# Kernel tuning notes

Hardware: AMD Instinct MI355X
Metric: run time of the kernel (lower is better)

## Reference

```python
import jax, jax.numpy as jnp
import numpy as np

N_FFT = 2048
HOP = 441
WIN_SIZE = 7
PAD = WIN_SIZE // 2
NP_WIN = WIN_SIZE * WIN_SIZE
COV_NORM = NP_WIN / (NP_WIN - 1.0)  # sample covariance, skimage default
DATA_RANGE = 2.0  # skimage float dtype_range (-1,1)
C1 = (0.01 * DATA_RANGE) ** 2
C2 = (0.03 * DATA_RANGE) ** 2
EPS = 1e-8

# periodic hann window (librosa fftbins=True)
_HANN = 0.5 - 0.5 * np.cos(2.0 * np.pi * np.arange(N_FFT) / N_FFT)


def wav_to_spectrogram(x):
    # x: [B, C, S] -> magnitude spectrogram [B, C, T, F]
    pad = N_FFT // 2
    xp = jnp.pad(x, ((0, 0), (0, 0), (pad, pad)), mode='reflect')  # torch 'reflect'
    L = xp.shape[-1]
    n_frames = (L - N_FFT) // HOP + 1
    idx = jnp.arange(n_frames)[:, None] * HOP + jnp.arange(N_FFT)[None, :]
    frames = xp[..., idx] * jnp.asarray(_HANN, xp.dtype)  # [B,C,T,N_FFT]
    spec = jnp.fft.rfft(frames, axis=-1)
    mag = jnp.sqrt(jnp.maximum(spec.real ** 2 + spec.imag ** 2, EPS))
    return mag


def _umean_last(x):
    # 1D uniform mean filter (size 7) along last axis, scipy 'reflect' boundary
    xp = jnp.pad(x, [(0, 0)] * (x.ndim - 1) + [(PAD, PAD)], mode='symmetric')
    cs = jnp.cumsum(xp, axis=-1)
    zero = jnp.zeros(cs.shape[:-1] + (1,), cs.dtype)
    cs = jnp.concatenate([zero, cs], axis=-1)
    return (cs[..., WIN_SIZE:] - cs[..., :-WIN_SIZE]) / WIN_SIZE


def umean2d(x):
    # separable 7x7 uniform filter over last two axes
    x = _umean_last(x)
    x = jnp.swapaxes(_umean_last(jnp.swapaxes(x, -1, -2)), -1, -2)
    return x


def ssim_map_mean(X, Y):
    ux, uy = umean2d(X), umean2d(Y)
    uxx, uyy, uxy = umean2d(X * X), umean2d(Y * Y), umean2d(X * Y)
    vx = COV_NORM * (uxx - ux * ux)
    vy = COV_NORM * (uyy - uy * uy)
    vxy = COV_NORM * (uxy - ux * uy)
    S = ((2 * ux * uy + C1) * (2 * vxy + C2)) / ((ux * ux + uy * uy + C1) * (vx + vy + C2))
    # crop pad on each side (skimage) then mean over the spatial map
    return jnp.mean(S[..., PAD:-PAD, PAD:-PAD], axis=(-2, -1))


def setup_inputs() -> dict:
    key = jax.random.key(0)
    k1, k2 = jax.random.split(key)
    B, C, S = 32, 2, 176400
    output = jax.random.normal(k1, (B, C, S), dtype=jnp.float32)
    target = jax.random.normal(k2, (B, C, S), dtype=jnp.float32)
    return {"output": output, "target": target}


def reference(output, target):
    so = wav_to_spectrogram(output)
    st = wav_to_spectrogram(target)
    res = ssim_map_mean(so, st)  # [B, C]
    return res[..., None, None]  # [B, C, 1, 1]
```

## Files before the change

### kernel.cpp

```cpp
#include <hip/hip_runtime.h>
#include <math.h>

#ifndef M_PI
#define M_PI 3.14159265358979323846
#endif

constexpr int S_LEN    = 176400;
constexpr int NFFT     = 2048;
constexpr int NC       = 1024;
constexpr int HOP_     = 441;
constexpr int T_FRAMES = 401;
constexpr int F_BINS   = 1025;
constexpr int F_STRIDE = 1028;
constexpr int N_CH     = 64;
constexpr float EPS_   = 1e-8f;
constexpr float C1_    = 0.0004f;
constexpr float C2_    = 0.0036f;
constexpr float COV_NORM_ = 49.0f / 48.0f;

constexpr int WIN_OFF  = 0;
constexpr int TWG_OFF  = 2048;
constexpr int UTW_OFF  = 3584;
constexpr int SPEC_OFF = 5696;
constexpr int RPB_     = 10;
constexpr int N_CHUNKS = 40;

__device__ __forceinline__ int phys(int i) { return i ^ ((i >> 2) & 15) ^ ((i >> 6) & 15); }

__device__ __forceinline__ float2 cadd(float2 a, float2 b){ return make_float2(a.x+b.x, a.y+b.y); }
__device__ __forceinline__ float2 csub(float2 a, float2 b){ return make_float2(a.x-b.x, a.y-b.y); }
__device__ __forceinline__ float2 cmul(float2 a, float2 b){ return make_float2(a.x*b.x-a.y*b.y, a.x*b.y+a.y*b.x); }

__global__ __launch_bounds__(256) void init_tables_kernel(float* __restrict__ ws, float* __restrict__ out) {
    const int idx = blockIdx.x * 256 + threadIdx.x;
    if (idx < 64) out[idx] = 0.0f;
    if (idx < NFFT) {
        ws[WIN_OFF + idx] = 0.5f - 0.5f * cosf((float)(2.0 * M_PI / NFFT) * (float)idx);
    }
    if (idx < 768) {
        float ang = -2.0f * (float)M_PI * (float)idx / (float)NC;
        float s, c; sincosf(ang, &s, &c);
        ws[TWG_OFF + 2*idx] = c; ws[TWG_OFF + 2*idx+1] = s;
    }
    if (idx < F_BINS) {
        float ang = -(float)M_PI * (float)idx / (float)NC;
        float s, c; sincosf(ang, &s, &c);
        ws[UTW_OFF + 2*idx] = c; ws[UTW_OFF + 2*idx+1] = s;
    }
}

__device__ __forceinline__ void r4_dif_inplace(
    float2* __restrict__ A, int r0, int r1, int r2, int r3,
    float2 w1, float2 w2, float2 w3, bool tw)
{
    float2 x0c = A[r0];
    float2 x1c = A[r1];
    float2 x2c = A[r2];
    float2 x3c = A[r3];

    float2 a = cadd(x0c, x2c);
    float2 b = csub(x0c, x2c);
    float2 c = cadd(x1c, x3c);
    float2 d = csub(x1c, x3c);

    float2 y0 = cadd(a, c);
    float2 y2 = csub(a, c);
    float2 y1 = make_float2(b.x + d.y, b.y - d.x);
    float2 y3 = make_float2(b.x - d.y, b.y + d.x);

    A[r0] = y0;
    A[r1] = tw ? cmul(y1, w1) : y1;
    A[r2] = tw ? cmul(y2, w2) : y2;
    A[r3] = tw ? cmul(y3, w3) : y3;
}

__global__ __launch_bounds__(256, 8) void stft_mag_kernel(
    const float* __restrict__ x0, const float* __restrict__ x1,
    float* __restrict__ ws, int ch0, int nch, int swizzle)
{
    __shared__ float2 buf[2 * NC];

    const int tid = threadIdx.x;

    int ch, t;
    if (swizzle) {
        int g = blockIdx.x;
        ch = ch0 + (g & 7) * 8 + ((g >> 3) & 7);
        t  = g >> 6;
    } else {
        t  = blockIdx.x;
        ch = ch0 + blockIdx.y;
    }

    const float* __restrict__ xin0 = x0 + (size_t)ch * S_LEN;
    const float* __restrict__ xin1 = x1 + (size_t)ch * S_LEN;
    const float*  __restrict__ win = ws + WIN_OFF;
    const float2* __restrict__ twg = (const float2*)(ws + TWG_OFF);
    const float2* __restrict__ utw = (const float2*)(ws + UTW_OFF);

    const int base = t * HOP_ - NFFT / 2;
    float* fA0 = (float*)buf;
    float* fA1 = (float*)(buf + NC);
    if (base >= 0 && base + NFFT <= S_LEN) {
        #pragma unroll
        for (int k = 0; k < NFFT / 256; ++k) {
            int n = k * 256 + tid;
            int j = base + n;
            float w = win[n];
            int p = 2 * phys(n >> 1) + (n & 1);
            fA0[p] = xin0[j] * w;
            fA1[p] = xin1[j] * w;
        }
    } else {
        #pragma unroll
        for (int k = 0; k < NFFT / 256; ++k) {
            int n = k * 256 + tid;
            int j = base + n;
            j = (j < 0) ? -j : j;
            j = (j >= S_LEN) ? (2 * S_LEN - 2 - j) : j;
            float w = win[n];
            int p = 2 * phys(n >> 1) + (n & 1);
            fA0[p] = xin0[j] * w;
            fA1[p] = xin1[j] * w;
        }
    }
    __syncthreads();

    #pragma unroll
    for (int s = 0; s < 5; ++s) {
        const int M  = 256 >> (2 * s);
        const int q  = tid & (M - 1);
        const int e  = q << (2 * s);
        const int i0 = 4 * (tid - q) + q;

        const int r0 = phys(i0);
        const int r1 = phys(i0 + M);
        const int r2 = phys(i0 + 2 * M);
        const int r3 = phys(i0 + 3 * M);

        float2 w1, w2, w3;
        if (s < 4) {
            w1 = twg[e];
            w2 = twg[2 * e];
            w3 = twg[3 * e];
        } else {
            w1 = w2 = w3 = make_float2(1.0f, 0.0f);
        }

        r4_dif_inplace(buf,      r0, r1, r2, r3, w1, w2, w3, s < 4);
        r4_dif_inplace(buf + NC, r0, r1, r2, r3, w1, w2, w3, s < 4);

        __syncthreads();
    }

    const size_t perT = (size_t)T_FRAMES * F_STRIDE;
    float* __restrict__ sout0 =
        ws + SPEC_OFF + (size_t)(ch - ch0) * perT + (size_t)t * F_STRIDE;
    float* __restrict__ sout1 = sout0 + (size_t)nch * perT;

    const int R8 = ((tid & 3) << 6) | ((tid & 12) << 2) | ((tid >> 2) & 12) | ((tid >> 6) & 3);

    #pragma unroll
    for (int k = 0; k < 5; ++k) {
        int r = k * 256 + tid;
        if (k < 4 || tid == 0) {
            const int ra = (k < 4) ? ((R8 << 2) | k) : 0;
            const int rn = (NC - r) & (NC - 1);
            const int rb = ((rn & 3) << 8) | ((rn & 12) << 4) | (rn & 48)
                         | ((rn >> 4) & 12) | ((rn >> 8) & 3);
            const int ia = phys(ra);
            const int ib = phys(rb);
            float2 wu = utw[r];

            {
                float2 Zr = buf[ia];
                float2 Zn = buf[ib];
                float Ex = 0.5f * (Zr.x + Zn.x);
                float Ey = 0.5f * (Zr.y - Zn.y);
                float Ox = 0.5f * (Zr.y + Zn.y);
                float Oy = 0.5f * (Zn.x - Zr.x);
                float Xx = Ex + wu.x * Ox - wu.y * Oy;
                float Xy = Ey + wu.x * Oy + wu.y * Ox;
                sout0[r] = sqrtf(fmaxf(Xx * Xx + Xy * Xy, EPS_));
            }
            {
                float2 Zr = buf[NC + ia];
                float2 Zn = buf[NC + ib];
                float Ex = 0.5f * (Zr.x + Zn.x);
                float Ey = 0.5f * (Zr.y - Zn.y);
                float Ox = 0.5f * (Zr.y + Zn.y);
                float Oy = 0.5f * (Zn.x - Zr.x);
                float Xx = Ex + wu.x * Ox - wu.y * Oy;
                float Xy = Ey + wu.x * Oy + wu.y * Ox;
                sout1[r] = sqrtf(fmaxf(Xx * Xx + Xy * Xy, EPS_));
            }
        }
    }
}

__global__ __launch_bounds__(256) void ssim_kernel(
    const float* __restrict__ ws, float* __restrict__ out,
    int ch0, int nch)
{
    __shared__ float csx[1284], csy[1284], csxx[1284], csyy[1284], csxy[1284];
    __shared__ double red[256];

    const int tid = threadIdx.x;
    const int cg  = blockIdx.y;
    const int ch  = ch0 + cg;
    const float* __restrict__ spec = ws + SPEC_OFF;
    const size_t per_ch = (size_t)T_FRAMES * F_STRIDE;
    const float* __restrict__ X = spec + (size_t)cg * per_ch;
    const float* __restrict__ Y = spec + ((size_t)nch + cg) * per_ch;

    const int t_begin = 3 + blockIdx.x * RPB_;
    const int t_end_  = min(t_begin + RPB_, T_FRAMES - 3);

    const int fv = tid << 2;
    const bool last = (tid == 255);
    const float inv49 = 1.0f / 49.0f;
    double acc = 0.0;

    float sx[4] = {0,0,0,0}, sy[4] = {0,0,0,0}, sxx[4] = {0,0,0,0},
          syy[4] = {0,0,0,0}, sxy[4] = {0,0,0,0};
    float s5[5] = {0,0,0,0,0};

    for (int rr = t_begin - 3; rr < t_begin + 3; ++rr) {
        float4 xv = *(const float4*)(X + (size_t)rr * F_STRIDE + fv);
        float4 yv = *(const float4*)(Y + (size_t)rr * F_STRIDE + fv);
        float xa[4] = {xv.x, xv.y, xv.z, xv.w}, ya[4] = {yv.x, yv.y, yv.z, yv.w};
        #pragma unroll
        for (int c = 0; c < 4; ++c) {
            sx[c] += xa[c]; sy[c] += ya[c];
            sxx[c] += xa[c]*xa[c]; syy[c] += ya[c]*ya[c]; sxy[c] += xa[c]*ya[c];
        }
        if (last) {
            float xe = X[(size_t)rr * F_STRIDE + 1024];
            float ye = Y[(size_t)rr * F_STRIDE + 1024];
            s5[0] += xe; s5[1] += ye; s5[2] += xe*xe; s5[3] += ye*ye; s5[4] += xe*ye;
        }
    }

    float4 ax, ay, bx, by; float a5x=0, a5y=0, b5x=0, b5y=0;
    ax = *(const float4*)(X + (size_t)(t_begin + 3) * F_STRIDE + fv);
    ay = *(const float4*)(Y + (size_t)(t_begin + 3) * F_STRIDE + fv);
    bx = *(const float4*)(X + (size_t)(t_begin - 3) * F_STRIDE + fv);
    by = *(const float4*)(Y + (size_t)(t_begin - 3) * F_STRIDE + fv);
    if (last) {
        a5x = X[(size_t)(t_begin + 3) * F_STRIDE + 1024];
        a5y = Y[(size_t)(t_begin + 3) * F_STRIDE + 1024];
        b5x = X[(size_t)(t_begin - 3) * F_STRIDE + 1024];
        b5y = Y[(size_t)(t_begin - 3) * F_STRIDE + 1024];
    }

    const int fo = 3 + (tid << 2);

    for (int t = t_begin; t < t_end_; ++t) {
        {
            float xa[4] = {ax.x, ax.y, ax.z, ax.w}, ya[4] = {ay.x, ay.y, ay.z, ay.w};
            #pragma unroll
            for (int c = 0; c < 4; ++c) {
                sx[c] += xa[c]; sy[c] += ya[c];
                sxx[c] += xa[c]*xa[c]; syy[c] += ya[c]*ya[c]; sxy[c] += xa[c]*ya[c];
                int p = 5 * tid + c;
                csx[p] = sx[c]; csy[p] = sy[c];
                csxx[p] = sxx[c]; csyy[p] = syy[c]; csxy[p] = sxy[c];
            }
            if (last) {
                s5[0] += a5x; s5[1] += a5y; s5[2] += a5x*a5x; s5[3] += a5y*a5y; s5[4] += a5x*a5y;
                csx[1280] = s5[0]; csy[1280] = s5[1];
                csxx[1280] = s5[2]; csyy[1280] = s5[3]; csxy[1280] = s5[4];
            }
        }
        __syncthreads();

        {
            float xa[4] = {bx.x, bx.y, bx.z, bx.w}, ya[4] = {by.x, by.y, by.z, by.w};
            #pragma unroll
            for (int c = 0; c < 4; ++c) {
                sx[c] -= xa[c]; sy[c] -= ya[c];
                sxx[c] -= xa[c]*xa[c]; syy[c] -= ya[c]*ya[c]; sxy[c] -= xa[c]*ya[c];
            }
            if (last) {
                s5[0] -= b5x; s5[1] -= b5y; s5[2] -= b5x*b5x; s5[3] -= b5y*b5y; s5[4] -= b5x*b5y;
            }
        }
        if (t + 1 < t_end_) {
            ax = *(const float4*)(X + (size_t)(t + 4) * F_STRIDE + fv);
            ay = *(const float4*)(Y + (size_t)(t + 4) * F_STRIDE + fv);
            bx = *(const float4*)(X + (size_t)(t - 2) * F_STRIDE + fv);
            by = *(const float4*)(Y + (size_t)(t - 2) * F_STRIDE + fv);
            if (last) {
                a5x = X[(size_t)(t + 4) * F_STRIDE + 1024];
                a5y = Y[(size_t)(t + 4) * F_STRIDE + 1024];
                b5x = X[(size_t)(t - 2) * F_STRIDE + 1024];
                b5y = Y[(size_t)(t - 2) * F_STRIDE + 1024];
            }
        }

        if (tid < 255) {
            float tx[10], ty[10], txx[10], tyy[10], txy[10];
            #pragma unroll
            for (int d = 0; d < 10; ++d) {
                int p = 5 * tid + d + (d >> 2);
                tx[d] = csx[p]; ty[d] = csy[p];
                txx[d] = csxx[p]; tyy[d] = csyy[p]; txy[d] = csxy[p];
            }
            float wx  = tx[0]+tx[1]+tx[2]+tx[3]+tx[4]+tx[5]+tx[6];
            float wy  = ty[0]+ty[1]+ty[2]+ty[3]+ty[4]+ty[5]+ty[6];
            float wxx = txx[0]+txx[1]+txx[2]+txx[3]+txx[4]+txx[5]+txx[6];
            float wyy = tyy[0]+tyy[1]+tyy[2]+tyy[3]+tyy[4]+tyy[5]+tyy[6];
            float wxy = txy[0]+txy[1]+txy[2]+txy[3]+txy[4]+txy[5]+txy[6];
            #pragma unroll
            for (int c = 0; c < 4; ++c) {
                if (fo + c <= 1021) {
                    float ux  = wx * inv49, uy  = wy * inv49;
                    float uxx = wxx * inv49, uyy = wyy * inv49, uxy = wxy * inv49;
                    float vx  = COV_NORM_ * (uxx - ux * ux);
                    float vy  = COV_NORM_ * (uyy - uy * uy);
                    float vxy = COV_NORM_ * (uxy - ux * uy);
                    float Sv = ((2.f * ux * uy + C1_) * (2.f * vxy + C2_)) /
                               ((ux * ux + uy * uy + C1_) * (vx + vy + C2_));
                    acc += (double)Sv;
                }
                if (c < 3) {
                    wx  += tx[c+7]  - tx[c];
                    wy  += ty[c+7]  - ty[c];
                    wxx += txx[c+7] - txx[c];
                    wyy += tyy[c+7] - tyy[c];
                    wxy += txy[c+7] - txy[c];
                }
            }
        }
        __syncthreads();
    }

    red[tid] = acc;
    __syncthreads();
    for (int off = 128; off > 0; off >>= 1) {
        if (tid < off) red[tid] += red[tid + off];
        __syncthreads();
    }
    if (tid == 0) {
        atomicAdd(&out[ch], (float)(red[0] / (395.0 * 1019.0)));
    }
}

extern "C" void kernel_launch(void* const* d_in, const int* in_sizes, int n_in,
                              void* d_out, int out_size, void* d_ws, size_t ws_size,
                              hipStream_t stream) {
    const float* x0 = (const float*)d_in[0];
    const float* x1 = (const float*)d_in[1];
    float* out = (float*)d_out;
    float* ws  = (float*)d_ws;

    const size_t table_bytes  = (size_t)SPEC_OFF * sizeof(float);
    const size_t per_ch_bytes = (size_t)2 * T_FRAMES * F_STRIDE * sizeof(float);
    int G = (int)((ws_size - table_bytes) / per_ch_bytes);
    if (G > N_CH) G = N_CH;
    if (G < 1)    G = 1;

    init_tables_kernel<<<dim3(16), dim3(256), 0, stream>>>(ws, out);

    for (int ch0 = 0; ch0 < N_CH; ch0 += G) {
        const int nch = (N_CH - ch0 < G) ? (N_CH - ch0) : G;

        if (nch == 64) {
            stft_mag_kernel<<<dim3(T_FRAMES * 64), dim3(256), 0, stream>>>(x0, x1, ws, ch0, nch, 1);
        } else {
            stft_mag_kernel<<<dim3(T_FRAMES, nch), dim3(256), 0, stream>>>(x0, x1, ws, ch0, nch, 0);
        }

        dim3 g2(N_CHUNKS, nch);
        ssim_kernel<<<g2, 256, 0, stream>>>(ws, out, ch0, nch);
    }
}
```

Measured before the change: 342.0 us.

## Make SSIM kernel wave-local with shuffle-based horizontal window sums

Reworks the SSIM kernel so each 64-lane wavefront independently handles a frequency band (overlapping by halo columns) and a chunk of time rows. The horizontal 7-tap box sum is computed with cross-lane shuffles instead of shared-memory column sums, removing the two block barriers per row and the LDS traffic, and the final reduction becomes a wave shuffle reduction. In exchange, overlapping bands re-read halo columns and re-accumulate more vertical warm-up rows, and the per-row prefetch of the next rows is dropped.

```diff
diff --git a/kernel.cpp b/kernel.cpp
--- a/kernel.cpp
+++ b/kernel.cpp
@@ -22,8 +22,11 @@
 constexpr int TWG_OFF  = 2048;
 constexpr int UTW_OFF  = 3584;
 constexpr int SPEC_OFF = 5696;
-constexpr int RPB_     = 10;
-constexpr int N_CHUNKS = 40;
+
+constexpr int ROWS_PW   = 16;
+constexpr int NCHUNKS_R = 25;
+constexpr int BANDS     = 5;
+constexpr int BAND_ADV  = 248;
 
 __device__ __forceinline__ int phys(int i) { return i ^ ((i >> 2) & 15) ^ ((i >> 6) & 15); }
 
@@ -198,151 +201,115 @@
     }
 }
 
+#define HWIN7(sarr, W) {                                                     \
+    float p0 = sarr[0], p01 = p0 + sarr[1], p012 = p01 + sarr[2],            \
+          P = p012 + sarr[3];                                                \
+    float a1 = __shfl_down(p012, 1, 64);                                     \
+    float A1 = __shfl_down(P,    1, 64);                                     \
+    float b0 = __shfl_down(p0,   2, 64);                                     \
+    float b1 = __shfl_down(p01,  2, 64);                                     \
+    W[0] = P + a1;                                                           \
+    W[1] = P - p0 + A1;                                                      \
+    W[2] = W[1] - sarr[1] + b0;                                              \
+    W[3] = W[2] - sarr[2] + (b1 - b0);                                       \
+}
+
 __global__ __launch_bounds__(256) void ssim_kernel(
     const float* __restrict__ ws, float* __restrict__ out,
     int ch0, int nch)
 {
-    __shared__ float csx[1284], csy[1284], csxx[1284], csyy[1284], csxy[1284];
-    __shared__ double red[256];
-
-    const int tid = threadIdx.x;
-    const int cg  = blockIdx.y;
-    const int ch  = ch0 + cg;
-    const float* __restrict__ spec = ws + SPEC_OFF;
-    const size_t per_ch = (size_t)T_FRAMES * F_STRIDE;
-    const float* __restrict__ X = spec + (size_t)cg * per_ch;
-    const float* __restrict__ Y = spec + ((size_t)nch + cg) * per_ch;
-
-    const int t_begin = 3 + blockIdx.x * RPB_;
-    const int t_end_  = min(t_begin + RPB_, T_FRAMES - 3);
-
-    const int fv = tid << 2;
-    const bool last = (tid == 255);
-    const float inv49 = 1.0f / 49.0f;
-    double acc = 0.0;
+    const int tid  = threadIdx.x;
+    const int wid  = blockIdx.x * 4 + (tid >> 6);
+    const int lane = tid & 63;
+    const int total = nch * BANDS * NCHUNKS_R;
+    if (wid >= total) return;
+
+    const int cg    = wid / (BANDS * NCHUNKS_R);
+    const int rem   = wid - cg * (BANDS * NCHUNKS_R);
+    const int band  = rem / NCHUNKS_R;
+    const int chunk = rem - band * NCHUNKS_R;
+
+    const int t0 = 3 + chunk * ROWS_PW;
+    const int t1 = min(t0 + ROWS_PW, T_FRAMES - 3);
+
+    const int cb = band * BAND_ADV;
+    int c4 = cb + 4 * lane;
+    if (c4 > 1024) c4 = 1024;
+
+    const size_t perT = (size_t)T_FRAMES * F_STRIDE;
+    const float* __restrict__ X = ws + SPEC_OFF + (size_t)cg * perT + c4;
+    const float* __restrict__ Y = ws + SPEC_OFF + ((size_t)nch + cg) * perT + c4;
+
+    const int  fo      = cb + 3 + 4 * lane;
+    const bool lane_ok = (lane <= 61);
+    const float inv49  = 1.0f / 49.0f;
 
     float sx[4] = {0,0,0,0}, sy[4] = {0,0,0,0}, sxx[4] = {0,0,0,0},
           syy[4] = {0,0,0,0}, sxy[4] = {0,0,0,0};
-    float s5[5] = {0,0,0,0,0};
-
-    for (int rr = t_begin - 3; rr < t_begin + 3; ++rr) {
-        float4 xv = *(const float4*)(X + (size_t)rr * F_STRIDE + fv);
-        float4 yv = *(const float4*)(Y + (size_t)rr * F_STRIDE + fv);
+
+    for (int rr = t0 - 3; rr < t0 + 3; ++rr) {
+        float4 xv = *(const float4*)(X + (size_t)rr * F_STRIDE);
+        float4 yv = *(const float4*)(Y + (size_t)rr * F_STRIDE);
         float xa[4] = {xv.x, xv.y, xv.z, xv.w}, ya[4] = {yv.x, yv.y, yv.z, yv.w};
         #pragma unroll
         for (int c = 0; c < 4; ++c) {
             sx[c] += xa[c]; sy[c] += ya[c];
             sxx[c] += xa[c]*xa[c]; syy[c] += ya[c]*ya[c]; sxy[c] += xa[c]*ya[c];
         }
-        if (last) {
-            float xe = X[(size_t)rr * F_STRIDE + 1024];
-            float ye = Y[(size_t)rr * F_STRIDE + 1024];
-            s5[0] += xe; s5[1] += ye; s5[2] += xe*xe; s5[3] += ye*ye; s5[4] += xe*ye;
-        }
-    }
-
-    float4 ax, ay, bx, by; float a5x=0, a5y=0, b5x=0, b5y=0;
-    ax = *(const float4*)(X + (size_t)(t_begin + 3) * F_STRIDE + fv);
-    ay = *(const float4*)(Y + (size_t)(t_begin + 3) * F_STRIDE + fv);
-    bx = *(const float4*)(X + (size_t)(t_begin - 3) * F_STRIDE + fv);
-    by = *(const float4*)(Y + (size_t)(t_begin - 3) * F_STRIDE + fv);
-    if (last) {
-        a5x = X[(size_t)(t_begin + 3) * F_STRIDE + 1024];
-        a5y = Y[(size_t)(t_begin + 3) * F_STRIDE + 1024];
-        b5x = X[(size_t)(t_begin - 3) * F_STRIDE + 1024];
-        b5y = Y[(size_t)(t_begin - 3) * F_STRIDE + 1024];
-    }
-
-    const int fo = 3 + (tid << 2);
-
-    for (int t = t_begin; t < t_end_; ++t) {
+    }
+
+    double acc = 0.0;
+
+    #pragma unroll 1
+    for (int t = t0; t < t1; ++t) {
         {
-            float xa[4] = {ax.x, ax.y, ax.z, ax.w}, ya[4] = {ay.x, ay.y, ay.z, ay.w};
+            float4 xv = *(const float4*)(X + (size_t)(t + 3) * F_STRIDE);
+            float4 yv = *(const float4*)(Y + (size_t)(t + 3) * F_STRIDE);
+            float xa[4] = {xv.x, xv.y, xv.z, xv.w}, ya[4] = {yv.x, yv.y, yv.z, yv.w};
             #pragma unroll
             for (int c = 0; c < 4; ++c) {
                 sx[c] += xa[c]; sy[c] += ya[c];
                 sxx[c] += xa[c]*xa[c]; syy[c] += ya[c]*ya[c]; sxy[c] += xa[c]*ya[c];
-                int p = 5 * tid + c;
-                csx[p] = sx[c]; csy[p] = sy[c];
-                csxx[p] = sxx[c]; csyy[p] = syy[c]; csxy[p] = sxy[c];
-            }
-            if (last) {
-                s5[0] += a5x; s5[1] += a5y; s5[2] += a5x*a5x; s5[3] += a5y*a5y; s5[4] += a5x*a5y;
-                csx[1280] = s5[0]; csy[1280] = s5[1];
-                csxx[1280] = s5[2]; csyy[1280] = s5[3]; csxy[1280] = s5[4];
-            }
-        }
-        __syncthreads();
+            }
+        }
+
+        float wx[4], wy[4], wxx[4], wyy[4], wxy[4];
+        HWIN7(sx,  wx);
+        HWIN7(sy,  wy);
+        HWIN7(sxx, wxx);
+        HWIN7(syy, wyy);
+        HWIN7(sxy, wxy);
+
+        #pragma unroll
+        for (int c = 0; c < 4; ++c) {
+            if (lane_ok && (fo + c <= 1021)) {
+                float ux  = wx[c]  * inv49, uy  = wy[c]  * inv49;
+                float uxx = wxx[c] * inv49, uyy = wyy[c] * inv49, uxy = wxy[c] * inv49;
+                float vx  = COV_NORM_ * (uxx - ux * ux);
+                float vy  = COV_NORM_ * (uyy - uy * uy);
+                float vxy = COV_NORM_ * (uxy - ux * uy);
+                float Sv = ((2.f * ux * uy + C1_) * (2.f * vxy + C2_)) /
+                           ((ux * ux + uy * uy + C1_) * (vx + vy + C2_));
+                acc += (double)Sv;
+            }
+        }
 
         {
-            float xa[4] = {bx.x, bx.y, bx.z, bx.w}, ya[4] = {by.x, by.y, by.z, by.w};
+            float4 xv = *(const float4*)(X + (size_t)(t - 3) * F_STRIDE);
+            float4 yv = *(const float4*)(Y + (size_t)(t - 3) * F_STRIDE);
+            float xa[4] = {xv.x, xv.y, xv.z, xv.w}, ya[4] = {yv.x, yv.y, yv.z, yv.w};
             #pragma unroll
             for (int c = 0; c < 4; ++c) {
                 sx[c] -= xa[c]; sy[c] -= ya[c];
                 sxx[c] -= xa[c]*xa[c]; syy[c] -= ya[c]*ya[c]; sxy[c] -= xa[c]*ya[c];
             }
-            if (last) {
-                s5[0] -= b5x; s5[1] -= b5y; s5[2] -= b5x*b5x; s5[3] -= b5y*b5y; s5[4] -= b5x*b5y;
-            }
-        }
-        if (t + 1 < t_end_) {
-            ax = *(const float4*)(X + (size_t)(t + 4) * F_STRIDE + fv);
-            ay = *(const float4*)(Y + (size_t)(t + 4) * F_STRIDE + fv);
-            bx = *(const float4*)(X + (size_t)(t - 2) * F_STRIDE + fv);
-            by = *(const float4*)(Y + (size_t)(t - 2) * F_STRIDE + fv);
-            if (last) {
-                a5x = X[(size_t)(t + 4) * F_STRIDE + 1024];
-                a5y = Y[(size_t)(t + 4) * F_STRIDE + 1024];
-                b5x = X[(size_t)(t - 2) * F_STRIDE + 1024];
-                b5y = Y[(size_t)(t - 2) * F_STRIDE + 1024];
-            }
-        }
-
-        if (tid < 255) {
-            float tx[10], ty[10], txx[10], tyy[10], txy[10];
-            #pragma unroll
-            for (int d = 0; d < 10; ++d) {
-                int p = 5 * tid + d + (d >> 2);
-                tx[d] = csx[p]; ty[d] = csy[p];
-                txx[d] = csxx[p]; tyy[d] = csyy[p]; txy[d] = csxy[p];
-            }
-            float wx  = tx[0]+tx[1]+tx[2]+tx[3]+tx[4]+tx[5]+tx[6];
-            float wy  = ty[0]+ty[1]+ty[2]+ty[3]+ty[4]+ty[5]+ty[6];
-            float wxx = txx[0]+txx[1]+txx[2]+txx[3]+txx[4]+txx[5]+txx[6];
-            float wyy = tyy[0]+tyy[1]+tyy[2]+tyy[3]+tyy[4]+tyy[5]+tyy[6];
-            float wxy = txy[0]+txy[1]+txy[2]+txy[3]+txy[4]+txy[5]+txy[6];
-            #pragma unroll
-            for (int c = 0; c < 4; ++c) {
-                if (fo + c <= 1021) {
-                    float ux  = wx * inv49, uy  = wy * inv49;
-                    float uxx = wxx * inv49, uyy = wyy * inv49, uxy = wxy * inv49;
-                    float vx  = COV_NORM_ * (uxx - ux * ux);
-                    float vy  = COV_NORM_ * (uyy - uy * uy);
-                    float vxy = COV_NORM_ * (uxy - ux * uy);
-                    float Sv = ((2.f * ux * uy + C1_) * (2.f * vxy + C2_)) /
-                               ((ux * ux + uy * uy + C1_) * (vx + vy + C2_));
-                    acc += (double)Sv;
-                }
-                if (c < 3) {
-                    wx  += tx[c+7]  - tx[c];
-                    wy  += ty[c+7]  - ty[c];
-                    wxx += txx[c+7] - txx[c];
-                    wyy += tyy[c+7] - tyy[c];
-                    wxy += txy[c+7] - txy[c];
-                }
-            }
-        }
-        __syncthreads();
-    }
-
-    red[tid] = acc;
-    __syncthreads();
-    for (int off = 128; off > 0; off >>= 1) {
-        if (tid < off) red[tid] += red[tid + off];
-        __syncthreads();
-    }
-    if (tid == 0) {
-        atomicAdd(&out[ch], (float)(red[0] / (395.0 * 1019.0)));
+        }
+    }
+
+    #pragma unroll
+    for (int off = 32; off > 0; off >>= 1) acc += __shfl_down(acc, off, 64);
+    if (lane == 0) {
+        atomicAdd(&out[ch0 + cg], (float)(acc / (395.0 * 1019.0)));
     }
 }
 
@@ -371,7 +338,7 @@
             stft_mag_kernel<<<dim3(T_FRAMES, nch), dim3(256), 0, stream>>>(x0, x1, ws, ch0, nch, 0);
         }
 
-        dim3 g2(N_CHUNKS, nch);
-        ssim_kernel<<<g2, 256, 0, stream>>>(ws, out, ch0, nch);
-    }
-}
+        const int nwaves = nch * BANDS * NCHUNKS_R;
+        ssim_kernel<<<dim3((nwaves + 3) / 4), dim3(256), 0, stream>>>(ws, out, ch0, nch);
+    }
+}
```

Result: slower. 370.8 us (+8.4%).
